# Optimization experiments

Measured on AMD Instinct MI355X. Metric: run time of the kernel, lower is better.

The kernel has to match this reference:

```python
import jax, jax.numpy as jnp
import numpy as np

N = 10000
E = 160000
IN_CH, HID, OUT = 14, 128, 4
HEADS = 8
NEG_SLOPE = 0.2


def setup_inputs() -> dict:
    key = jax.random.key(0)
    ks = jax.random.split(key, 16)
    glorot = lambda k, shape: jax.random.normal(k, shape, jnp.float32) * np.sqrt(2.0 / (shape[0] + shape[-1]))
    inp = {
        'x': jax.random.normal(ks[0], (N, IN_CH), jnp.float32),
        'edge_index': jax.random.randint(ks[1], (2, E), 0, N, jnp.int64),
        # layer 1: 14 -> 8 heads x 128, concat
        'W1': glorot(ks[2], (IN_CH, HEADS * HID)),
        'a_src1': glorot(ks[3], (HEADS, HID)),
        'a_dst1': glorot(ks[4], (HEADS, HID)),
        'b1': jnp.zeros((HEADS * HID,), jnp.float32),
        # layer 2: 1024 -> 8 heads x 128, concat
        'W2': glorot(ks[5], (HEADS * HID, HEADS * HID)),
        'a_src2': glorot(ks[6], (HEADS, HID)),
        'a_dst2': glorot(ks[7], (HEADS, HID)),
        'b2': jnp.zeros((HEADS * HID,), jnp.float32),
        # layer 3: 1024 -> 1 head x 4, mean (concat=False)
        'W3': glorot(ks[8], (HEADS * HID, OUT)),
        'a_src3': glorot(ks[9], (1, OUT)),
        'a_dst3': glorot(ks[10], (1, OUT)),
        'b3': jnp.zeros((OUT,), jnp.float32),
    }
    return inp


def gat_conv(x, src, dst, W, a_src, a_dst, b, heads, out_ch, concat):
    n = x.shape[0]
    h = (x @ W).reshape(n, heads, out_ch)                      # [N,H,C]
    al_s = jnp.sum(h * a_src, axis=-1)                         # [N,H]
    al_d = jnp.sum(h * a_dst, axis=-1)                         # [N,H]
    e = al_s[src] + al_d[dst]                                  # [E,H]
    e = jnp.where(e > 0, e, NEG_SLOPE * e)                     # LeakyReLU(0.2)
    # segment softmax over incoming edges of each dst node
    m = jax.ops.segment_max(e, dst, num_segments=n)
    ex = jnp.exp(e - m[dst])
    z = jax.ops.segment_sum(ex, dst, num_segments=n)
    alpha = ex / (z[dst] + 1e-16)                              # [E,H]
    out = jax.ops.segment_sum(h[src] * alpha[:, :, None], dst, num_segments=n)  # [N,H,C]
    out = out.reshape(n, heads * out_ch) if concat else out.mean(axis=1)
    return out + b


def reference(x, edge_index, W1, a_src1, a_dst1, b1, W2, a_src2, a_dst2, b2, W3, a_src3, a_dst3, b3):
    n = x.shape[0]
    # add self-loops (PyG GATConv default)
    loop = jnp.arange(n, dtype=edge_index.dtype)
    src = jnp.concatenate([edge_index[0], loop])
    dst = jnp.concatenate([edge_index[1], loop])
    # dropout layers are identity in eval mode
    h = gat_conv(x, src, dst, W1, a_src1, a_dst1, b1, HEADS, HID, True)
    h = jax.nn.relu(h)
    h = gat_conv(h, src, dst, W2, a_src2, a_dst2, b2, HEADS, HID, True)
    h = jax.nn.relu(h)
    h = gat_conv(h, src, dst, W3, a_src3, a_dst3, b3, 1, OUT, False)
    h = jax.nn.relu(h)
    return h
```

## Files before the change

kernel.cpp:

```cpp
#include <hip/hip_runtime.h>

typedef unsigned short ushort_t;
typedef unsigned int uint32;

#define N_NODES 10000
#define N_EDGES 160000
#define ET (N_NODES + N_EDGES)
#define MPAD 10112
#define HT 1024
#define HEADS 8
#define NEG 0.2f

#define O_FLAG     0
#define O_SRC      256
#define O_DST      (O_SRC + 680192)
#define O_COUNTS   (O_DST + 680192)
#define O_OFFS     (O_COUNTS + 40192)
#define O_CURS     (O_OFFS + 40192)
#define O_SSORT    (O_CURS + 40192)
#define O_ALS      (O_SSORT + 680192)
#define O_ALD      (O_ALS + 320000)
#define O_AL3S     (O_ALD + 320000)
#define O_AL3D     (O_AL3S + 40192)
#define O_H3       (O_AL3D + 40192)
#define O_XF       (O_H3 + 160000)
#define O_W1F      (O_XF + 560128)
#define O_AS1F     (O_W1F + 57344)
#define O_W3F      (O_AS1F + 24576)
#define O_S3F      (O_W3F + 16384)
#define O_W2T      (O_S3F + 768)
#define O_BUFA     (O_W2T + 2097152)
#define O_BUFB     (O_BUFA + 20709376)

__device__ __forceinline__ float bf2f(ushort_t u){ return __uint_as_float(((uint32)u) << 16); }
__device__ __forceinline__ ushort_t f2bf(float f){
    uint32 x = __float_as_uint(f);
    return (ushort_t)((x + 0x7fffu + ((x >> 16) & 1u)) >> 16);
}
__device__ __forceinline__ void unpack2(uint32 u, float& lo, float& hi){
    lo = __uint_as_float(u << 16);
    hi = __uint_as_float(u & 0xffff0000u);
}

typedef __bf16 bf16x8 __attribute__((ext_vector_type(8)));
typedef float  f32x4  __attribute__((ext_vector_type(4)));

typedef const __attribute__((address_space(1))) uint32* gas1_u32;
typedef       __attribute__((address_space(3))) uint32* las3_u32;

__device__ __forceinline__ void gload_lds16(const void* g, void* l){
    __builtin_amdgcn_global_load_lds((gas1_u32)g, (las3_u32)l, 16, 0, 0);
}

__device__ __forceinline__ int probe_f32(const uint32* __restrict__ w){
    int cnt = 0;
    for (int i = 0; i < 256; i++){
        uint32 e = (w[i] >> 7) & 0xffu;
        cnt += (e >= 64u && e <= 160u) ? 1 : 0;
    }
    return (cnt > 200) ? 0 : 1;
}
__device__ __forceinline__ int probe_edge64(const int* __restrict__ ei){
    int nz = 0;
    for (int i = 0; i < 128; i++) nz |= ei[2*i + 1];
    return (nz == 0) ? 1 : 0;
}

struct CvtArgs {
    const void* src[12];
    float*      dst[12];
    int         n[12];
};

__global__ __launch_bounds__(256) void k_setup(CvtArgs a, const void* __restrict__ W2,
                                               const uint32* __restrict__ w1raw,
                                               const int* __restrict__ eiraw,
                                               int* __restrict__ counts,
                                               ushort_t* __restrict__ W2T,
                                               int* __restrict__ flags){
    __shared__ ushort_t tile[32][33];
    int slice = blockIdx.y;
    int tid = threadIdx.x;
    if (slice < 12){
        int n = a.n[slice];
        int base = blockIdx.x * 1024 + tid * 4;
        if (base >= n) return;
        int f32 = probe_f32(w1raw);
        const void* s = a.src[slice];
        float* d = a.dst[slice];
        #pragma unroll
        for (int j = 0; j < 4; j++){
            int i = base + j;
            if (i < n) d[i] = f32 ? ((const float*)s)[i] : bf2f(((const ushort_t*)s)[i]);
        }
    } else if (slice == 12){
        if (blockIdx.x == 10){
            if (tid == 0) flags[0] = probe_edge64(eiraw);
            if (tid == 1) flags[1] = probe_f32(w1raw);
            return;
        }
        if (blockIdx.x < 10){
            int i0 = blockIdx.x * 1024 + tid * 4;
            if (i0 + 3 < N_NODES){
                *(int4*)(counts + i0) = make_int4(0,0,0,0);
            } else {
                for (int j = 0; j < 4; j++) if (i0 + j < N_NODES) counts[i0 + j] = 0;
            }
        }
    } else {
        int f32 = probe_f32(w1raw);
        int bx = blockIdx.x & 31, by = blockIdx.x >> 5;
        int cx = tid & 31;
        int ry = (tid >> 5) * 4;
        #pragma unroll
        for (int r = 0; r < 4; r++){
            size_t idx = (size_t)(by*32 + ry + r)*1024 + bx*32 + cx;
            tile[ry + r][cx] = f32 ? f2bf(((const float*)W2)[idx]) : ((const ushort_t*)W2)[idx];
        }
        __syncthreads();
        #pragma unroll
        for (int r = 0; r < 4; r++)
            W2T[(size_t)(bx*32 + ry + r)*1024 + by*32 + cx] = tile[cx][ry + r];
    }
}

__global__ __launch_bounds__(256) void k_extract_hist(const void* __restrict__ ei, const int* __restrict__ flags,
                                                      int* __restrict__ src, int* __restrict__ dst,
                                                      int* __restrict__ counts){
    int i = blockIdx.x * 256 + threadIdx.x;
    int is64 = flags[0];
    int s = -1, d = -1;
    if (i < N_EDGES){
        if (is64){
            const long long* p = (const long long*)ei;
            s = (int)p[i]; d = (int)p[N_EDGES + i];
        } else {
            const int* p = (const int*)ei;
            s = p[i]; d = p[N_EDGES + i];
        }
    } else if (i < ET){
        s = i - N_EDGES; d = s;
    }
    if (d >= 0){
        src[i] = s; dst[i] = d;
        atomicAdd(&counts[d], 1);
    }
}

__global__ __launch_bounds__(1024) void k_scan(const int* __restrict__ counts, int* __restrict__ offs,
                                               int* __restrict__ cursors, int n){
    __shared__ int wsum[16];
    __shared__ int running_s;
    int tid = threadIdx.x;
    int lane = tid & 63, wid = tid >> 6;
    if (tid == 0) running_s = 0;
    __syncthreads();
    for (int base = 0; base < n; base += 1024){
        int i = base + tid;
        int v = (i < n) ? counts[i] : 0;
        int x = v;
        #pragma unroll
        for (int d = 1; d < 64; d <<= 1){
            int t = __shfl_up(x, d, 64);
            if (lane >= d) x += t;
        }
        if (lane == 63) wsum[wid] = x;
        __syncthreads();
        if (wid == 0 && lane < 16){
            int w = wsum[lane];
            #pragma unroll
            for (int d = 1; d < 16; d <<= 1){
                int t = __shfl_up(w, d, 64);
                if (lane >= d) w += t;
            }
            wsum[lane] = w;
        }
        __syncthreads();
        int wprefix = (wid == 0) ? 0 : wsum[wid - 1];
        int run = running_s;
        int excl = run + wprefix + (x - v);
        if (i < n){ offs[i] = excl; cursors[i] = excl; }
        __syncthreads();
        if (tid == 0) running_s = run + wsum[15];
        __syncthreads();
    }
    if (tid == 0) offs[n] = running_s;
}

__global__ __launch_bounds__(256) void k_scatter(const int* __restrict__ src, const int* __restrict__ dst,
                                                 int* __restrict__ cursors, int* __restrict__ ssort){
    int i = blockIdx.x * 256 + threadIdx.x;
    if (i < ET){
        int pos = atomicAdd(&cursors[dst[i]], 1);
        ssort[pos] = src[i];
    }
}

__global__ __launch_bounds__(256) void k_gemm1f(const float* __restrict__ x, const float* __restrict__ W1,
                                                const float* __restrict__ a_src, const float* __restrict__ a_dst,
                                                ushort_t* __restrict__ h1,
                                                float* __restrict__ alS, float* __restrict__ alD){
    __shared__ float w1s[14 * HT];
    int tid = threadIdx.x;
    for (int i = tid * 4; i < 14 * HT; i += 1024)
        *(float4*)(w1s + i) = *(const float4*)(W1 + i);
    int c0 = tid * 4;
    float4 sv = *(const float4*)(a_src + c0);
    float4 dv = *(const float4*)(a_dst + c0);
    int head = tid >> 5, l32 = tid & 31;
    __syncthreads();
    for (int n = blockIdx.x; n < N_NODES; n += gridDim.x){
        float a0=0.f, a1=0.f, a2=0.f, a3=0.f;
        #pragma unroll
        for (int k = 0; k < 14; k++){
            float xv = x[n*14 + k];
            float4 w = *(const float4*)(w1s + k*HT + c0);
            a0 += xv*w.x; a1 += xv*w.y; a2 += xv*w.z; a3 += xv*w.w;
        }
        uint2 o;
        o.x = (uint32)f2bf(a0) | ((uint32)f2bf(a1) << 16);
        o.y = (uint32)f2bf(a2) | ((uint32)f2bf(a3) << 16);
        *(uint2*)(h1 + (size_t)n*HT + c0) = o;
        float h0,h1v,h2,h3v;
        unpack2(o.x, h0, h1v); unpack2(o.y, h2, h3v);
        float s = h0*sv.x + h1v*sv.y + h2*sv.z + h3v*sv.w;
        float d = h0*dv.x + h1v*dv.y + h2*dv.z + h3v*dv.w;
        #pragma unroll
        for (int of = 16; of; of >>= 1){ s += __shfl_xor(s, of, 32); d += __shfl_xor(d, of, 32); }
        if (l32 == 0){ alS[n*HEADS + head] = s; alD[n*HEADS + head] = d; }
    }
}

__global__ __launch_bounds__(256) void k_gat_agg(const ushort_t* __restrict__ H, const float* __restrict__ alS,
                                                 const float* __restrict__ alD, const int* __restrict__ offs,
                                                 const int* __restrict__ srcs, const float* __restrict__ bias,
                                                 ushort_t* __restrict__ out){
    int tid = threadIdx.x;
    int wv = tid >> 6, lane = tid & 63;
    int n = blockIdx.x * 2 + (wv >> 1);
    int half = wv & 1;
    int beg = offs[n], end = offs[n+1];
    int head = half*4 + (lane >> 4);
    int slot = lane & 15;
    float ad = alD[n*HEADS + head];

    float m = -1e30f, z = 0.f;
    for (int c = beg; c < end; c += 64){
        int cn = min(64, end - c);
        int sreg = (lane < cn) ? srcs[c + lane] : 0;
        for (int p = slot; p < cn; p += 16){
            int s = __shfl(sreg, p, 64);
            float v = alS[s*HEADS + head] + ad;
            v = v > 0.f ? v : NEG*v;
            if (v > m){ z = z*__expf(m - v) + 1.f; m = v; }
            else z += __expf(v - m);
        }
    }
    #pragma unroll
    for (int o = 1; o < 16; o <<= 1){
        float m2 = __shfl_xor(m, o, 64);
        float z2 = __shfl_xor(z, o, 64);
        float nm = fmaxf(m, m2);
        z = z*__expf(m - nm) + z2*__expf(m2 - nm);
        m = nm;
    }
    float inv = 1.f / (z + 1e-16f);

    int ch0 = half*512 + lane*8;
    const ushort_t* Hc = H + ch0;
    float c0=0.f,c1=0.f,c2=0.f,c3=0.f,c4=0.f,c5=0.f,c6=0.f,c7=0.f;
    for (int c = beg; c < end; c += 64){
        int cn = min(64, end - c);
        int sreg = (lane < cn) ? srcs[c + lane] : 0;
        int j = 0;
        for (; j + 4 <= cn; j += 4){
            int s0 = __shfl(sreg, j, 64);
            int s1 = __shfl(sreg, j+1, 64);
            int s2 = __shfl(sreg, j+2, 64);
            int s3 = __shfl(sreg, j+3, 64);
            float e0 = alS[s0*HEADS + head];
            float e1 = alS[s1*HEADS + head];
            float e2 = alS[s2*HEADS + head];
            float e3 = alS[s3*HEADS + head];
            uint4 u0 = *(const uint4*)(Hc + (size_t)s0*HT);
            uint4 u1 = *(const uint4*)(Hc + (size_t)s1*HT);
            uint4 u2 = *(const uint4*)(Hc + (size_t)s2*HT);
            uint4 u3 = *(const uint4*)(Hc + (size_t)s3*HT);
            float v0 = e0 + ad; v0 = v0 > 0.f ? v0 : NEG*v0;
            float v1 = e1 + ad; v1 = v1 > 0.f ? v1 : NEG*v1;
            float v2 = e2 + ad; v2 = v2 > 0.f ? v2 : NEG*v2;
            float v3 = e3 + ad; v3 = v3 > 0.f ? v3 : NEG*v3;
            float w0 = __expf(v0 - m) * inv;
            float w1 = __expf(v1 - m) * inv;
            float w2 = __expf(v2 - m) * inv;
            float w3 = __expf(v3 - m) * inv;
            float f0,f1,f2,f3,f4,f5,f6,f7;
            unpack2(u0.x,f0,f1); unpack2(u0.y,f2,f3); unpack2(u0.z,f4,f5); unpack2(u0.w,f6,f7);
            c0+=w0*f0; c1+=w0*f1; c2+=w0*f2; c3+=w0*f3;
            c4+=w0*f4; c5+=w0*f5; c6+=w0*f6; c7+=w0*f7;
            unpack2(u1.x,f0,f1); unpack2(u1.y,f2,f3); unpack2(u1.z,f4,f5); unpack2(u1.w,f6,f7);
            c0+=w1*f0; c1+=w1*f1; c2+=w1*f2; c3+=w1*f3;
            c4+=w1*f4; c5+=w1*f5; c6+=w1*f6; c7+=w1*f7;
            unpack2(u2.x,f0,f1); unpack2(u2.y,f2,f3); unpack2(u2.z,f4,f5); unpack2(u2.w,f6,f7);
            c0+=w2*f0; c1+=w2*f1; c2+=w2*f2; c3+=w2*f3;
            c4+=w2*f4; c5+=w2*f5; c6+=w2*f6; c7+=w2*f7;
            unpack2(u3.x,f0,f1); unpack2(u3.y,f2,f3); unpack2(u3.z,f4,f5); unpack2(u3.w,f6,f7);
            c0+=w3*f0; c1+=w3*f1; c2+=w3*f2; c3+=w3*f3;
            c4+=w3*f4; c5+=w3*f5; c6+=w3*f6; c7+=w3*f7;
        }
        for (; j < cn; j++){
            int s0 = __shfl(sreg, j, 64);
            uint4 u0 = *(const uint4*)(Hc + (size_t)s0*HT);
            float v0 = alS[s0*HEADS + head] + ad;
            v0 = v0 > 0.f ? v0 : NEG*v0;
            float w0 = __expf(v0 - m) * inv;
            float f0,f1,f2,f3,f4,f5,f6,f7;
            unpack2(u0.x,f0,f1); unpack2(u0.y,f2,f3); unpack2(u0.z,f4,f5); unpack2(u0.w,f6,f7);
            c0+=w0*f0; c1+=w0*f1; c2+=w0*f2; c3+=w0*f3;
            c4+=w0*f4; c5+=w0*f5; c6+=w0*f6; c7+=w0*f7;
        }
    }
    float4 b0 = *(const float4*)(bias + ch0);
    float4 b1 = *(const float4*)(bias + ch0 + 4);
    c0 = fmaxf(c0+b0.x, 0.f); c1 = fmaxf(c1+b0.y, 0.f);
    c2 = fmaxf(c2+b0.z, 0.f); c3 = fmaxf(c3+b0.w, 0.f);
    c4 = fmaxf(c4+b1.x, 0.f); c5 = fmaxf(c5+b1.y, 0.f);
    c6 = fmaxf(c6+b1.z, 0.f); c7 = fmaxf(c7+b1.w, 0.f);
    uint4 o;
    o.x = (uint32)f2bf(c0) | ((uint32)f2bf(c1) << 16);
    o.y = (uint32)f2bf(c2) | ((uint32)f2bf(c3) << 16);
    o.z = (uint32)f2bf(c4) | ((uint32)f2bf(c5) << 16);
    o.w = (uint32)f2bf(c6) | ((uint32)f2bf(c7) << 16);
    *(uint4*)(out + (size_t)n*HT + ch0) = o;
}

__global__ __launch_bounds__(256) void k_gemm2(const ushort_t* __restrict__ A, const ushort_t* __restrict__ BT,
                                               ushort_t* __restrict__ C,
                                               const float* __restrict__ aS, const float* __restrict__ aD,
                                               float* __restrict__ alS, float* __restrict__ alD){
    __shared__ ushort_t lbuf[2][2][128*64];
    float (*reds)[64][2] = (float (*)[64][2])lbuf;
    int L = blockIdx.x;
    int xcd = L & 7;
    int wi  = L >> 3;
    int bm  = xcd * 10 + (wi >> 3);
    int bn  = wi & 7;
    if (bm >= 79) return;
    int tid = threadIdx.x;
    int lane = tid & 63;
    int wave = tid >> 6;
    int wm = (wave & 1) * 64, wn = (wave >> 1) * 64;
    int lm = lane & 15, kg = lane >> 4;
    int c0 = (kg ^ (lm & 7)) * 8;
    f32x4 acc[4][4];
    #pragma unroll
    for (int i = 0; i < 4; i++)
        #pragma unroll
        for (int j = 0; j < 4; j++) acc[i][j] = (f32x4)0.0f;

    const int K = 1024;
    int rowA0 = bm * 128, rowB0 = bn * 128;

    auto stage = [&](int buf, int k0){
        #pragma unroll
        for (int it = 0; it < 4; ++it){
            int s = tid + it*256;
            int r = s >> 3;
            int q = (s & 7) ^ (r & 7);
            gload_lds16(A  + (size_t)(rowA0 + r)*K + k0 + q*8, &lbuf[buf][0][s*8]);
            gload_lds16(BT + (size_t)(rowB0 + r)*K + k0 + q*8, &lbuf[buf][1][s*8]);
        }
    };

    stage(0, 0);
    asm volatile("s_waitcnt vmcnt(0)" ::: "memory");
    __syncthreads();
    int cur = 0;
    for (int k0 = 0; k0 < K; k0 += 64){
        if (k0 + 64 < K) stage(cur ^ 1, k0 + 64);
        bf16x8 a0[4], a1[4], b0[4], b1[4];
        #pragma unroll
        for (int mt = 0; mt < 4; mt++){
            const ushort_t* base = &lbuf[cur][0][(wm + mt*16 + lm)*64];
            a0[mt] = *(const bf16x8*)(base + c0);
            a1[mt] = *(const bf16x8*)(base + (c0 ^ 32));
        }
        #pragma unroll
        for (int nt = 0; nt < 4; nt++){
            const ushort_t* base = &lbuf[cur][1][(wn + nt*16 + lm)*64];
            b0[nt] = *(const bf16x8*)(base + c0);
            b1[nt] = *(const bf16x8*)(base + (c0 ^ 32));
        }
        #pragma unroll
        for (int mt = 0; mt < 4; mt++)
            #pragma unroll
            for (int nt = 0; nt < 4; nt++)
                acc[mt][nt] = __builtin_amdgcn_mfma_f32_16x16x32_bf16(a0[mt], b0[nt], acc[mt][nt], 0, 0, 0);
        #pragma unroll
        for (int mt = 0; mt < 4; mt++)
            #pragma unroll
            for (int nt = 0; nt < 4; nt++)
                acc[mt][nt] = __builtin_amdgcn_mfma_f32_16x16x32_bf16(a1[mt], b1[nt], acc[mt][nt], 0, 0, 0);
        asm volatile("s_waitcnt vmcnt(0)" ::: "memory");
        __syncthreads();
        cur ^= 1;
    }
    #pragma unroll
    for (int mt = 0; mt < 4; mt++){
        int row_base = bm*128 + wm + mt*16 + kg*4;
        #pragma unroll
        for (int nt = 0; nt < 4; nt++){
            int col = bn*128 + wn + nt*16 + lm;
            #pragma unroll
            for (int r = 0; r < 4; r++){
                int row = row_base + r;
                if (row < N_NODES) C[(size_t)row*HT + col] = f2bf(acc[mt][nt][r]);
            }
        }
    }
    float as_l[4], ad_l[4];
    #pragma unroll
    for (int nt = 0; nt < 4; nt++){
        as_l[nt] = aS[bn*128 + wn + nt*16 + lm];
        ad_l[nt] = aD[bn*128 + wn + nt*16 + lm];
    }
    float psA[4][4], pdA[4][4];
    #pragma unroll
    for (int mt = 0; mt < 4; mt++){
        #pragma unroll
        for (int r = 0; r < 4; r++){
            float ps = acc[mt][0][r]*as_l[0] + acc[mt][1][r]*as_l[1]
                     + acc[mt][2][r]*as_l[2] + acc[mt][3][r]*as_l[3];
            float pd = acc[mt][0][r]*ad_l[0] + acc[mt][1][r]*ad_l[1]
                     + acc[mt][2][r]*ad_l[2] + acc[mt][3][r]*ad_l[3];
            #pragma unroll
            for (int o = 1; o < 16; o <<= 1){ ps += __shfl_xor(ps, o, 64); pd += __shfl_xor(pd, o, 64); }
            psA[mt][r] = ps; pdA[mt][r] = pd;
            if (wn == 64 && lm == 0){
                int rl = mt*16 + kg*4 + r;
                reds[wm >> 6][rl][0] = ps;
                reds[wm >> 6][rl][1] = pd;
            }
        }
    }
    __syncthreads();
    if (wn == 0 && lm == 0){
        #pragma unroll
        for (int mt = 0; mt < 4; mt++){
            #pragma unroll
            for (int r = 0; r < 4; r++){
                int rl = mt*16 + kg*4 + r;
                int row = bm*128 + wm + rl;
                if (row < N_NODES){
                    alS[row*HEADS + bn] = psA[mt][r] + reds[wm >> 6][rl][0];
                    alD[row*HEADS + bn] = pdA[mt][r] + reds[wm >> 6][rl][1];
                }
            }
        }
    }
}

__global__ __launch_bounds__(256) void k_gemm3(const ushort_t* __restrict__ A, const float* __restrict__ W3,
                                               const float* __restrict__ s3,
                                               float* __restrict__ h3, float* __restrict__ al3s, float* __restrict__ al3d){
    int tid = threadIdx.x;
    int lane = tid & 63, wave = tid >> 6;
    int n = blockIdx.x * 4 + wave;
    if (n >= N_NODES) return;
    float4 w3r[16];
    #pragma unroll
    for (int j = 0; j < 16; j++) w3r[j] = ((const float4*)W3)[lane*16 + j];
    const uint4* ap = (const uint4*)(A + (size_t)n*HT + lane*16);
    uint4 u0 = ap[0], u1 = ap[1];
    uint32 uu[8] = {u0.x,u0.y,u0.z,u0.w,u1.x,u1.y,u1.z,u1.w};
    float acc0=0.f, acc1=0.f, acc2=0.f, acc3=0.f;
    #pragma unroll
    for (int p = 0; p < 8; p++){
        float lo, hi;
        unpack2(uu[p], lo, hi);
        float4 wl = w3r[p*2], wh = w3r[p*2+1];
        acc0 += lo*wl.x + hi*wh.x;
        acc1 += lo*wl.y + hi*wh.y;
        acc2 += lo*wl.z + hi*wh.z;
        acc3 += lo*wl.w + hi*wh.w;
    }
    #pragma unroll
    for (int o = 32; o; o >>= 1){
        acc0 += __shfl_xor(acc0, o, 64); acc1 += __shfl_xor(acc1, o, 64);
        acc2 += __shfl_xor(acc2, o, 64); acc3 += __shfl_xor(acc3, o, 64);
    }
    if (lane == 0){
        *(float4*)(h3 + n*4) = make_float4(acc0, acc1, acc2, acc3);
        al3s[n] = acc0*s3[0] + acc1*s3[1] + acc2*s3[2] + acc3*s3[3];
        al3d[n] = acc0*s3[16] + acc1*s3[17] + acc2*s3[18] + acc3*s3[19];
    }
}

__global__ __launch_bounds__(256) void k_gat_agg3(const float* __restrict__ h3, const float* __restrict__ al3s,
                                                  const float* __restrict__ al3d, const int* __restrict__ offs,
                                                  const int* __restrict__ srcs, const float* __restrict__ b3,
                                                  const int* __restrict__ flags, void* __restrict__ out){
    int tid = threadIdx.x;
    int l = tid & 63, wave = tid >> 6;
    int n = blockIdx.x * 4 + wave;
    if (n >= N_NODES) return;
    int beg = offs[n], end = offs[n+1];
    float ad = al3d[n];
    float m = -1e30f;
    for (int e = beg + l; e < end; e += 64){
        float v = al3s[srcs[e]] + ad; v = v > 0.f ? v : NEG*v;
        m = fmaxf(m, v);
    }
    #pragma unroll
    for (int o = 32; o; o >>= 1) m = fmaxf(m, __shfl_xor(m, o, 64));
    float z = 0.f;
    for (int e = beg + l; e < end; e += 64){
        float v = al3s[srcs[e]] + ad; v = v > 0.f ? v : NEG*v;
        z += __expf(v - m);
    }
    #pragma unroll
    for (int o = 32; o; o >>= 1) z += __shfl_xor(z, o, 64);
    float inv = 1.f / (z + 1e-16f);
    float a0=0.f, a1=0.f, a2=0.f, a3=0.f;
    for (int e = beg + l; e < end; e += 64){
        int s = srcs[e];
        float v = al3s[s] + ad; v = v > 0.f ? v : NEG*v;
        float w = __expf(v - m) * inv;
        float4 hv = *(const float4*)(h3 + s*4);
        a0 += w*hv.x; a1 += w*hv.y; a2 += w*hv.z; a3 += w*hv.w;
    }
    #pragma unroll
    for (int o = 32; o; o >>= 1){
        a0 += __shfl_xor(a0, o, 64); a1 += __shfl_xor(a1, o, 64);
        a2 += __shfl_xor(a2, o, 64); a3 += __shfl_xor(a3, o, 64);
    }
    if (l == 0){
        float r0 = fmaxf(a0 + b3[0], 0.f);
        float r1 = fmaxf(a1 + b3[1], 0.f);
        float r2 = fmaxf(a2 + b3[2], 0.f);
        float r3 = fmaxf(a3 + b3[3], 0.f);
        if (flags[1]){
            float* o4 = (float*)out;
            o4[n*4+0]=r0; o4[n*4+1]=r1; o4[n*4+2]=r2; o4[n*4+3]=r3;
        } else {
            ushort_t* o2 = (ushort_t*)out;
            o2[n*4+0]=f2bf(r0); o2[n*4+1]=f2bf(r1); o2[n*4+2]=f2bf(r2); o2[n*4+3]=f2bf(r3);
        }
    }
}

extern "C" void kernel_launch(void* const* d_in, const int* in_sizes, int n_in,
                              void* d_out, int out_size, void* d_ws, size_t ws_size,
                              hipStream_t stream){
    const void* x   = d_in[0];
    const void* ei  = d_in[1];
    const void* W1  = d_in[2];
    const void* as1 = d_in[3];
    const void* ad1 = d_in[4];
    const void* b1  = d_in[5];
    const void* W2  = d_in[6];
    const void* as2 = d_in[7];
    const void* ad2 = d_in[8];
    const void* b2  = d_in[9];
    const void* W3  = d_in[10];
    const void* as3 = d_in[11];
    const void* ad3 = d_in[12];
    const void* b3  = d_in[13];

    char* ws = (char*)d_ws;
    int* flags     = (int*)(ws + O_FLAG);
    int* srcA      = (int*)(ws + O_SRC);
    int* dstA      = (int*)(ws + O_DST);
    int* counts    = (int*)(ws + O_COUNTS);
    int* offs      = (int*)(ws + O_OFFS);
    int* cursors   = (int*)(ws + O_CURS);
    int* ssort     = (int*)(ws + O_SSORT);
    float* alS     = (float*)(ws + O_ALS);
    float* alD     = (float*)(ws + O_ALD);
    float* al3s    = (float*)(ws + O_AL3S);
    float* al3d    = (float*)(ws + O_AL3D);
    float* h3      = (float*)(ws + O_H3);
    float* xF      = (float*)(ws + O_XF);
    float* W1F     = (float*)(ws + O_W1F);
    float* wvecF   = (float*)(ws + O_AS1F);
    float* W3F     = (float*)(ws + O_W3F);
    float* s3F     = (float*)(ws + O_S3F);
    ushort_t* W2T  = (ushort_t*)(ws + O_W2T);
    ushort_t* bufA = (ushort_t*)(ws + O_BUFA);
    ushort_t* bufB = (ushort_t*)(ws + O_BUFB);

    const int EB = (ET + 255) / 256;

    CvtArgs ca;
    ca.src[0]=x;   ca.dst[0]=xF;            ca.n[0]=140000;
    ca.src[1]=W1;  ca.dst[1]=W1F;           ca.n[1]=14336;
    ca.src[2]=as1; ca.dst[2]=wvecF+0*1024;  ca.n[2]=1024;
    ca.src[3]=ad1; ca.dst[3]=wvecF+1*1024;  ca.n[3]=1024;
    ca.src[4]=b1;  ca.dst[4]=wvecF+2*1024;  ca.n[4]=1024;
    ca.src[5]=as2; ca.dst[5]=wvecF+3*1024;  ca.n[5]=1024;
    ca.src[6]=ad2; ca.dst[6]=wvecF+4*1024;  ca.n[6]=1024;
    ca.src[7]=b2;  ca.dst[7]=wvecF+5*1024;  ca.n[7]=1024;
    ca.src[8]=W3;  ca.dst[8]=W3F;           ca.n[8]=4096;
    ca.src[9]=as3; ca.dst[9]=s3F+0;         ca.n[9]=4;
    ca.src[10]=ad3; ca.dst[10]=s3F+16;      ca.n[10]=4;
    ca.src[11]=b3;  ca.dst[11]=s3F+32;      ca.n[11]=4;

    k_setup<<<dim3(1024, 14), 256, 0, stream>>>(ca, W2, (const uint32*)W1, (const int*)ei,
                                                counts, W2T, flags);
    k_extract_hist<<<EB, 256, 0, stream>>>(ei, flags, srcA, dstA, counts);
    k_scan<<<1, 1024, 0, stream>>>(counts, offs, cursors, N_NODES);
    k_scatter<<<EB, 256, 0, stream>>>(srcA, dstA, cursors, ssort);

    k_gemm1f<<<512, 256, 0, stream>>>(xF, W1F, wvecF+0*1024, wvecF+1*1024, bufA, alS, alD);
    k_gat_agg<<<5000, 256, 0, stream>>>(bufA, alS, alD, offs, ssort, wvecF+2*1024, bufB);

    k_gemm2<<<640, 256, 0, stream>>>(bufB, W2T, bufA, wvecF+3*1024, wvecF+4*1024, alS, alD);
    k_gat_agg<<<5000, 256, 0, stream>>>(bufA, alS, alD, offs, ssort, wvecF+5*1024, bufB);

    k_gemm3<<<2500, 256, 0, stream>>>(bufB, W3F, s3F, h3, al3s, al3d);
    k_gat_agg3<<<2500, 256, 0, stream>>>(h3, al3s, al3d, offs, ssort, s3F+32, flags, d_out);
}
```

Baseline: 318.3 us.

## Fuse softmax statistics into aggregation pass with online rescaling

Removes the separate first pass over each node's incoming edges that computed the segment max and sum. The aggregation loop now keeps a running max and denominator, rescaling the accumulators whenever a new max appears, and normalizes once at the end. This saves one sweep of index and alS gathers per node, at the cost of extra exp and multiply work on rescale events. The Hc loads are also issued before the alS loads.

```diff
diff --git a/kernel.cpp b/kernel.cpp
--- a/kernel.cpp
+++ b/kernel.cpp
@@ -241,33 +241,11 @@
     int half = wv & 1;
     int beg = offs[n], end = offs[n+1];
     int head = half*4 + (lane >> 4);
-    int slot = lane & 15;
     float ad = alD[n*HEADS + head];
-
-    float m = -1e30f, z = 0.f;
-    for (int c = beg; c < end; c += 64){
-        int cn = min(64, end - c);
-        int sreg = (lane < cn) ? srcs[c + lane] : 0;
-        for (int p = slot; p < cn; p += 16){
-            int s = __shfl(sreg, p, 64);
-            float v = alS[s*HEADS + head] + ad;
-            v = v > 0.f ? v : NEG*v;
-            if (v > m){ z = z*__expf(m - v) + 1.f; m = v; }
-            else z += __expf(v - m);
-        }
-    }
-    #pragma unroll
-    for (int o = 1; o < 16; o <<= 1){
-        float m2 = __shfl_xor(m, o, 64);
-        float z2 = __shfl_xor(z, o, 64);
-        float nm = fmaxf(m, m2);
-        z = z*__expf(m - nm) + z2*__expf(m2 - nm);
-        m = nm;
-    }
-    float inv = 1.f / (z + 1e-16f);
 
     int ch0 = half*512 + lane*8;
     const ushort_t* Hc = H + ch0;
+    float m = -1e30f, z = 0.f;
     float c0=0.f,c1=0.f,c2=0.f,c3=0.f,c4=0.f,c5=0.f,c6=0.f,c7=0.f;
     for (int c = beg; c < end; c += 64){
         int cn = min(64, end - c);
@@ -278,22 +256,31 @@
             int s1 = __shfl(sreg, j+1, 64);
             int s2 = __shfl(sreg, j+2, 64);
             int s3 = __shfl(sreg, j+3, 64);
+            uint4 u0 = *(const uint4*)(Hc + (size_t)s0*HT);
+            uint4 u1 = *(const uint4*)(Hc + (size_t)s1*HT);
+            uint4 u2 = *(const uint4*)(Hc + (size_t)s2*HT);
+            uint4 u3 = *(const uint4*)(Hc + (size_t)s3*HT);
             float e0 = alS[s0*HEADS + head];
             float e1 = alS[s1*HEADS + head];
             float e2 = alS[s2*HEADS + head];
             float e3 = alS[s3*HEADS + head];
-            uint4 u0 = *(const uint4*)(Hc + (size_t)s0*HT);
-            uint4 u1 = *(const uint4*)(Hc + (size_t)s1*HT);
-            uint4 u2 = *(const uint4*)(Hc + (size_t)s2*HT);
-            uint4 u3 = *(const uint4*)(Hc + (size_t)s3*HT);
             float v0 = e0 + ad; v0 = v0 > 0.f ? v0 : NEG*v0;
             float v1 = e1 + ad; v1 = v1 > 0.f ? v1 : NEG*v1;
             float v2 = e2 + ad; v2 = v2 > 0.f ? v2 : NEG*v2;
             float v3 = e3 + ad; v3 = v3 > 0.f ? v3 : NEG*v3;
-            float w0 = __expf(v0 - m) * inv;
-            float w1 = __expf(v1 - m) * inv;
-            float w2 = __expf(v2 - m) * inv;
-            float w3 = __expf(v3 - m) * inv;
+            float vm = fmaxf(fmaxf(v0, v1), fmaxf(v2, v3));
+            if (vm > m){
+                float sc = __expf(m - vm);
+                z *= sc;
+                c0*=sc; c1*=sc; c2*=sc; c3*=sc;
+                c4*=sc; c5*=sc; c6*=sc; c7*=sc;
+                m = vm;
+            }
+            float w0 = __expf(v0 - m);
+            float w1 = __expf(v1 - m);
+            float w2 = __expf(v2 - m);
+            float w3 = __expf(v3 - m);
+            z += (w0 + w1) + (w2 + w3);
             float f0,f1,f2,f3,f4,f5,f6,f7;
             unpack2(u0.x,f0,f1); unpack2(u0.y,f2,f3); unpack2(u0.z,f4,f5); unpack2(u0.w,f6,f7);
             c0+=w0*f0; c1+=w0*f1; c2+=w0*f2; c3+=w0*f3;
@@ -313,19 +300,28 @@
             uint4 u0 = *(const uint4*)(Hc + (size_t)s0*HT);
             float v0 = alS[s0*HEADS + head] + ad;
             v0 = v0 > 0.f ? v0 : NEG*v0;
-            float w0 = __expf(v0 - m) * inv;
+            if (v0 > m){
+                float sc = __expf(m - v0);
+                z *= sc;
+                c0*=sc; c1*=sc; c2*=sc; c3*=sc;
+                c4*=sc; c5*=sc; c6*=sc; c7*=sc;
+                m = v0;
+            }
+            float w0 = __expf(v0 - m);
+            z += w0;
             float f0,f1,f2,f3,f4,f5,f6,f7;
             unpack2(u0.x,f0,f1); unpack2(u0.y,f2,f3); unpack2(u0.z,f4,f5); unpack2(u0.w,f6,f7);
             c0+=w0*f0; c1+=w0*f1; c2+=w0*f2; c3+=w0*f3;
             c4+=w0*f4; c5+=w0*f5; c6+=w0*f6; c7+=w0*f7;
         }
     }
+    float inv = 1.f / (z + 1e-16f);
     float4 b0 = *(const float4*)(bias + ch0);
     float4 b1 = *(const float4*)(bias + ch0 + 4);
-    c0 = fmaxf(c0+b0.x, 0.f); c1 = fmaxf(c1+b0.y, 0.f);
-    c2 = fmaxf(c2+b0.z, 0.f); c3 = fmaxf(c3+b0.w, 0.f);
-    c4 = fmaxf(c4+b1.x, 0.f); c5 = fmaxf(c5+b1.y, 0.f);
-    c6 = fmaxf(c6+b1.z, 0.f); c7 = fmaxf(c7+b1.w, 0.f);
+    c0 = fmaxf(c0*inv+b0.x, 0.f); c1 = fmaxf(c1*inv+b0.y, 0.f);
+    c2 = fmaxf(c2*inv+b0.z, 0.f); c3 = fmaxf(c3*inv+b0.w, 0.f);
+    c4 = fmaxf(c4*inv+b1.x, 0.f); c5 = fmaxf(c5*inv+b1.y, 0.f);
+    c6 = fmaxf(c6*inv+b1.z, 0.f); c7 = fmaxf(c7*inv+b1.w, 0.f);
     uint4 o;
     o.x = (uint32)f2bf(c0) | ((uint32)f2bf(c1) << 16);
     o.y = (uint32)f2bf(c2) | ((uint32)f2bf(c3) << 16);
```

Result: no change. 318.2 us (-0.1%).
